# Kernel tuning notes

Hardware: AMD Instinct MI355X
Metric: run time of the kernel (lower is better)

Reference implementation:

```python
import jax, jax.numpy as jnp
import numpy as np

B, T, E = 2, 2048, 2048
H, HKV, M = 16, 4, 4
HD = E // H // M          # 32
NREP = H // HKV           # 4
EPS = 1e-5


def _rotary_interleaved(x, cos, sin):
    # x: (B, S, nh, HD); cos/sin: (S, HD//2), interleaved pairs (0::2, 1::2)
    x1 = x[..., 0::2]
    x2 = x[..., 1::2]
    c = cos[None, :, None, :]
    s = sin[None, :, None, :]
    o1 = x1 * c - x2 * s
    o2 = x1 * s + x2 * c
    return jnp.stack([o1, o2], axis=-1).reshape(x.shape)


def setup_inputs() -> dict:
    key = jax.random.key(0)
    ks = jax.random.split(key, 6)
    x = jax.random.normal(ks[0], (B, T, E), jnp.float32)
    pos = jnp.arange(T, dtype=jnp.float32)
    inv_freq = 1.0 / (10000.0 ** (jnp.arange(0, HD, 2, dtype=jnp.float32) / HD))
    ang = pos[:, None] * inv_freq[None, :]  # (T, HD//2)
    cos = jnp.cos(ang)
    sin = jnp.sin(ang)
    s = 0.02
    q_w = jax.random.normal(ks[1], (E, E), jnp.float32) * s
    k_w = jax.random.normal(ks[2], (E // NREP, E), jnp.float32) * s
    v_w = jax.random.normal(ks[3], (E // NREP, E), jnp.float32) * s
    out_w = jax.random.normal(ks[4], (E, E), jnp.float32) * s
    raw_map_weights = jnp.array([0.1 * (-1.0) ** i for i in range(M)], jnp.float32)
    weight_scale = jnp.ones((1,), jnp.float32)
    gamma = jnp.ones((M * HD,), jnp.float32)
    return dict(x=x, cos=cos, sin=sin, q_w=q_w, k_w=k_w, v_w=v_w, out_w=out_w,
                raw_map_weights=raw_map_weights, weight_scale=weight_scale, gamma=gamma)


def reference(x, cos, sin, q_w, k_w, v_w, out_w, raw_map_weights, weight_scale, gamma):
    # projections
    q = (x @ q_w.T).reshape(B, T, M * H, HD)
    k = (x @ k_w.T).reshape(B, T, M * HKV, HD)
    v = (x @ v_w.T).reshape(B, T, HKV, M * HD)
    # rotary (interleaved) on full head_dim, then split heads x maps (heads major, maps minor)
    q = _rotary_interleaved(q, cos, sin).reshape(B, T, H, M, HD)
    k = _rotary_interleaved(k, cos, sin).reshape(B, T, HKV, M, HD)
    # GQA: q head h attends to kv head h // NREP  (repeat_interleave semantics)
    k_rep = jnp.repeat(k, NREP, axis=2)  # (B,T,H,M,HD)
    v_rep = jnp.repeat(v, NREP, axis=2)  # (B,T,H,M*HD)
    map_w = jnp.tanh(raw_map_weights) * weight_scale[0]
    scale = HD ** -0.5  # flash_attn default softmax scale
    causal = jnp.tril(jnp.ones((T, T), dtype=bool))
    combined = jnp.zeros((B, T, H, M * HD), x.dtype)
    for i in range(M):  # small fixed num_maps loop
        scores = jnp.einsum('bqhd,bkhd->bhqk', q[:, :, :, i], k_rep[:, :, :, i]) * scale
        scores = jnp.where(causal[None, None], scores, -jnp.inf)
        p = jax.nn.softmax(scores, axis=-1)
        attn_i = jnp.einsum('bhqk,bkhe->bqhe', p, v_rep)  # (B,T,H,M*HD)
        combined = combined + map_w[i] * attn_i
    # RMSNorm over last dim (num_maps * head_dim) with affine weight
    var = jnp.mean(combined * combined, axis=-1, keepdims=True)
    normed = combined * jax.lax.rsqrt(var + EPS) * gamma
    out = normed.reshape(B, T, E) @ out_w.T
    return out
```

## Files before the change

kernel.cpp:

```cpp
#include <hip/hip_runtime.h>


typedef unsigned short u16;
typedef unsigned int u32;
typedef _Float16 f16;
typedef _Float16 f16x8 __attribute__((ext_vector_type(8)));
typedef float f32x4 __attribute__((ext_vector_type(4)));

#define B_ 2
#define T_ 2048
#define E_ 2048
#define H_ 16
#define HKV_ 4
#define M_ 4
#define HD_ 32
#define SCALE_Q 0.2550348873f

#define GLOAD_LDS(g, l)                                                   \
  __builtin_amdgcn_global_load_lds(                                       \
      (const __attribute__((address_space(1))) u32*)(g),                  \
      (__attribute__((address_space(3))) u32*)(l), 16, 0, 0)

__device__ __forceinline__ u16 f2h(float f) {
  f16 h = (f16)f;
  return __builtin_bit_cast(u16, h);
}

__global__ void cvt_all(const float* __restrict__ x, const float* __restrict__ qw,
                        const float* __restrict__ kw, const float* __restrict__ vw,
                        const float* __restrict__ ow, u16* __restrict__ xb,
                        u16* __restrict__ wcat, u16* __restrict__ wo16) {
  const float* src;
  u16* dst;
  int n4;
  switch (blockIdx.y) {
    case 0: src = x;  dst = xb;            n4 = 2097152; break;
    case 1: src = qw; dst = wcat;          n4 = 1048576; break;
    case 2: src = kw; dst = wcat + 4194304; n4 = 262144; break;
    case 3: src = vw; dst = wcat + 5242880; n4 = 262144; break;
    default: src = ow; dst = wo16;         n4 = 1048576; break;
  }
  int i = blockIdx.x * blockDim.x + threadIdx.x;
  if (i < n4) {
    float4 v = ((const float4*)src)[i];
    ushort4 o;
    o.x = f2h(v.x); o.y = f2h(v.y); o.z = f2h(v.z); o.w = f2h(v.w);
    ((ushort4*)dst)[i] = o;
  }
}

#define GEMM_CORE(A_, B_ptr, K_)                                              \
  for (int k0 = 0; k0 < (K_); k0 += 32) {                                     \
    _Pragma("unroll") for (int j = 0; j < 2; ++j) {                           \
      GLOAD_LDS(&(A_)[(size_t)(m0 + r0 + j * 64) * (K_) + k0 + c8],           \
                &As[tid * 8 + j * 2048]);                                     \
      GLOAD_LDS(&(B_ptr)[(size_t)(n0 + r0 + j * 64) * (K_) + k0 + c8],        \
                &Bs[tid * 8 + j * 2048]);                                     \
    }                                                                         \
    __syncthreads();                                                          \
    f16x8 af[4], bfr[4];                                                      \
    _Pragma("unroll") for (int mt = 0; mt < 4; ++mt)                          \
        af[mt] = *(const f16x8*)&As[(wm + mt * 16 + r) * 32 + g * 8];         \
    _Pragma("unroll") for (int nt = 0; nt < 4; ++nt)                          \
        bfr[nt] = *(const f16x8*)&Bs[(wn + nt * 16 + r) * 32 + g * 8];        \
    _Pragma("unroll") for (int mt = 0; mt < 4; ++mt)                          \
        _Pragma("unroll") for (int nt = 0; nt < 4; ++nt)                      \
            acc[mt][nt] = __builtin_amdgcn_mfma_f32_16x16x32_f16(             \
                af[mt], bfr[nt], acc[mt][nt], 0, 0, 0);                       \
    __syncthreads();                                                          \
  }

__global__ __launch_bounds__(256) void gemm_bt(const u16* __restrict__ A,
                                               const u16* __restrict__ Bm,
                                               float* __restrict__ C,
                                               int M, int N, int K) {
  __shared__ __align__(16) u16 As[128 * 32];
  __shared__ __align__(16) u16 Bs[128 * 32];
  const int tid = threadIdx.x;
  const int lane = tid & 63;
  const int wv = tid >> 6;
  const int g = lane >> 4;
  const int r = lane & 15;
  const int m0 = blockIdx.y * 128;
  const int n0 = blockIdx.x * 128;
  const int wm = (wv >> 1) * 64;
  const int wn = (wv & 1) * 64;
  f32x4 acc[4][4];
#pragma unroll
  for (int a = 0; a < 4; ++a)
#pragma unroll
    for (int b = 0; b < 4; ++b) acc[a][b] = (f32x4){0.f, 0.f, 0.f, 0.f};
  const int r0 = tid >> 2;
  const int c8 = (tid & 3) << 3;

  GEMM_CORE(A, Bm, K)

#pragma unroll
  for (int mt = 0; mt < 4; ++mt)
#pragma unroll
    for (int nt = 0; nt < 4; ++nt) {
      int row = m0 + wm + mt * 16 + g * 4;
      int col = n0 + wn + nt * 16 + r;
#pragma unroll
      for (int rr = 0; rr < 4; ++rr)
        C[(size_t)(row + rr) * N + col] = acc[mt][nt][rr];
    }
}

__global__ __launch_bounds__(256) void gemm_qkv_rope(
    const u16* __restrict__ A, const u16* __restrict__ Bm,
    const float* __restrict__ cosb, const float* __restrict__ sinb,
    u16* __restrict__ qp, u16* __restrict__ kp, u16* __restrict__ vtp) {
  __shared__ __align__(16) u16 As[128 * 32];
  __shared__ __align__(16) u16 Bs[128 * 32];
  const int tid = threadIdx.x;
  const int lane = tid & 63;
  const int wv = tid >> 6;
  const int g = lane >> 4;
  const int r = lane & 15;
  const int m0 = blockIdx.y * 128;
  const int n0 = blockIdx.x * 128;
  const int wm = (wv >> 1) * 64;
  const int wn = (wv & 1) * 64;
  f32x4 acc[4][4];
#pragma unroll
  for (int a = 0; a < 4; ++a)
#pragma unroll
    for (int b = 0; b < 4; ++b) acc[a][b] = (f32x4){0.f, 0.f, 0.f, 0.f};
  const int r0 = tid >> 2;
  const int c8 = (tid & 3) << 3;

  GEMM_CORE(A, Bm, 2048)

  const int b = m0 >> 11;
  const float signf = (r & 1) ? 1.f : -1.f;
  const int jb = r >> 1;

  if (n0 < 2048) {
#pragma unroll
    for (int mt = 0; mt < 4; ++mt) {
      int row = m0 + wm + mt * 16 + g * 4;
      int t0 = row & 2047;
#pragma unroll
      for (int rr = 0; rr < 4; ++rr) {
        int t = t0 + rr;
        float c0 = cosb[t * 16 + jb], s0 = sinb[t * 16 + jb];
        float c1 = cosb[t * 16 + 8 + jb], s1 = sinb[t * 16 + 8 + jb];
#pragma unroll
        for (int nt = 0; nt < 4; ++nt) {
          float xv = acc[mt][nt][rr];
          float pv = __shfl_xor(xv, 1, 64);
          float c = (nt & 1) ? c1 : c0;
          float s = (nt & 1) ? s1 : s0;
          float o = (xv * c + signf * pv * s) * SCALE_Q;
          int col = n0 + wn + nt * 16 + r;
          int hh = col >> 7, mm = (col >> 5) & 3, d = col & 31;
          qp[((((size_t)b * H_ + hh) * M_ + mm) * T_ + t) * HD_ + d] = f2h(o);
        }
      }
    }
  } else if (n0 < 2560) {
#pragma unroll
    for (int mt = 0; mt < 4; ++mt) {
      int row = m0 + wm + mt * 16 + g * 4;
      int t0 = row & 2047;
#pragma unroll
      for (int rr = 0; rr < 4; ++rr) {
        int t = t0 + rr;
        float c0 = cosb[t * 16 + jb], s0 = sinb[t * 16 + jb];
        float c1 = cosb[t * 16 + 8 + jb], s1 = sinb[t * 16 + 8 + jb];
#pragma unroll
        for (int nt = 0; nt < 4; ++nt) {
          float xv = acc[mt][nt][rr];
          float pv = __shfl_xor(xv, 1, 64);
          float c = (nt & 1) ? c1 : c0;
          float s = (nt & 1) ? s1 : s0;
          float o = xv * c + signf * pv * s;
          int col2 = n0 + wn + nt * 16 + r - 2048;
          int hh = col2 >> 7, mm = (col2 >> 5) & 3, d = col2 & 31;
          kp[((((size_t)b * HKV_ + hh) * M_ + mm) * T_ + t) * HD_ + d] = f2h(o);
        }
      }
    }
  } else {
#pragma unroll
    for (int mt = 0; mt < 4; ++mt) {
      int row = m0 + wm + mt * 16 + g * 4;
      int t0 = row & 2047;
#pragma unroll
      for (int nt = 0; nt < 4; ++nt) {
        int col3 = n0 + wn + nt * 16 + r - 2560;
        int hkv = col3 >> 7, e = col3 & 127;
        ushort4 w;
        w.x = f2h(acc[mt][nt][0]);
        w.y = f2h(acc[mt][nt][1]);
        w.z = f2h(acc[mt][nt][2]);
        w.w = f2h(acc[mt][nt][3]);
        *(ushort4*)&vtp[(((size_t)b * HKV_ + hkv) * 128 + e) * T_ + t0] = w;
      }
    }
  }
}

__global__ __launch_bounds__(256) void lstats_kernel(
    const u16* __restrict__ qp, const u16* __restrict__ kp,
    const float* __restrict__ rawW, const float* __restrict__ wscale,
    float* __restrict__ invw) {
  const int tid = threadIdx.x;
  const int lane = tid & 63;
  const int wv = tid >> 6;
  const int g = lane >> 4, r = lane & 15;
  const int h = blockIdx.y;
  const int b = blockIdx.z >> 2, e = blockIdx.z & 3;
  const int hkv = h >> 2;
  const int s0 = blockIdx.x * 4 + wv;

  const size_t qb = (((size_t)b * H_ + h) * M_ + e) * T_ * HD_;
  const size_t kb = (((size_t)b * HKV_ + hkv) * M_ + e) * T_ * HD_;
  const float mw = tanhf(rawW[e]) * wscale[0];

  for (int ps = 0; ps < 2; ++ps) {
    const int strip = ps ? 127 - s0 : s0;
    const int q0 = strip * 16;
    f16x8 qf = *(const f16x8*)&qp[qb + (size_t)(q0 + r) * HD_ + g * 8];
    float lacc[4] = {0.f, 0.f, 0.f, 0.f};

    for (int k0 = 0; k0 < q0 + 16; k0 += 64) {
      f32x4 s[4];
#pragma unroll
      for (int nt = 0; nt < 4; ++nt) {
        f16x8 kf = *(const f16x8*)&kp[kb + (size_t)(k0 + nt * 16 + r) * HD_ + g * 8];
        s[nt] = __builtin_amdgcn_mfma_f32_16x16x32_f16(qf, kf, (f32x4){0.f, 0.f, 0.f, 0.f}, 0, 0, 0);
      }
#pragma unroll
      for (int rr = 0; rr < 4; ++rr) {
        int row = q0 + g * 4 + rr;
#pragma unroll
        for (int nt = 0; nt < 4; ++nt) {
          int col = k0 + nt * 16 + r;
          float sv = (col <= row) ? s[nt][rr] : -1e30f;
          lacc[rr] += exp2f(sv);
        }
      }
    }
#pragma unroll
    for (int rr = 0; rr < 4; ++rr) {
      float l = lacc[rr];
#pragma unroll
      for (int off = 8; off >= 1; off >>= 1) l += __shfl_xor(l, off, 64);
      if (r == 0)
        invw[(((size_t)b * H_ + h) * M_ + e) * T_ + q0 + g * 4 + rr] = mw / l;
    }
  }
}

__global__ __launch_bounds__(256) void attn_kernel(
    const u16* __restrict__ qp, const u16* __restrict__ kp,
    const u16* __restrict__ vtp, const float* __restrict__ invw,
    const float* __restrict__ gamma, u16* __restrict__ normed) {
  __shared__ __align__(16) char smem[41984];
  u16* Ks = (u16*)smem;
  u16* Pc = (u16*)(smem + 32768);
  float* comb = (float*)smem;

  const int tid = threadIdx.x;
  const int lane = tid & 63;
  const int wv = tid >> 6;
  const int g = lane >> 4;
  const int r = lane & 15;
  const int h = blockIdx.y;
  const int b = blockIdx.z;
  const int hkv = h >> 2;

  const size_t qb = ((size_t)b * H_ + h) * M_ * T_ * HD_;
  const size_t kb = ((size_t)b * HKV_ + hkv) * M_ * T_ * HD_;
  const size_t vb = ((size_t)b * HKV_ + hkv) * 128 * (size_t)T_;

#define STAGE_KS(K0, DST)                                                     \
  {                                                                           \
    _Pragma("unroll") for (int j = 0; j < 4; ++j) {                           \
      int f = tid + j * 256;                                                  \
      int e_ = f >> 8, g2 = (f >> 6) & 3, kk = f & 63;                        \
      GLOAD_LDS(&kp[kb + ((size_t)e_ * T_ + (K0) + kk) * HD_ + g2 * 8],       \
                &(DST)[f * 8]);                                               \
    }                                                                         \
  }

  for (int ps = 0; ps < 2; ++ps) {
    const int q0 = (ps ? 31 - blockIdx.x : blockIdx.x) * 64;
    const int rq = q0 + wv * 16;

    f16x8 qf[4];
    float iw[4][4];
#pragma unroll
    for (int e = 0; e < 4; ++e) {
      qf[e] = *(const f16x8*)&qp[qb + ((size_t)e * T_ + rq + r) * HD_ + g * 8];
      const float* ivp = invw + (((size_t)b * H_ + h) * M_ + e) * T_;
#pragma unroll
      for (int rr = 0; rr < 4; ++rr) iw[e][rr] = ivp[rq + g * 4 + rr];
    }

    f32x4 acc[8];
#pragma unroll
    for (int ct = 0; ct < 8; ++ct) acc[ct] = (f32x4){0.f, 0.f, 0.f, 0.f};

    __syncthreads();
    STAGE_KS(0, Ks);
    __syncthreads();

    const int niter = q0 / 64 + 1;
    for (int i = 0; i < niter; ++i) {
      const int k0 = i * 64;
      u16* kbuf = Ks + (size_t)(i & 1) * 8192;
      if (i + 1 < niter) STAGE_KS(k0 + 64, Ks + (size_t)((i + 1) & 1) * 8192);

      f16x8 vf[2][8];
#pragma unroll
      for (int ct = 0; ct < 8; ++ct)
#pragma unroll
        for (int k2 = 0; k2 < 2; ++k2)
          vf[k2][ct] = *(const f16x8*)&vtp[vb + (size_t)(ct * 16 + r) * T_ + k0 + k2 * 32 + g * 8];

      float pc[4][4];
#pragma unroll
      for (int nt = 0; nt < 4; ++nt)
#pragma unroll
        for (int rr = 0; rr < 4; ++rr) pc[nt][rr] = 0.f;
      const bool need_mask = (k0 + 63 > rq);
#pragma unroll
      for (int e = 0; e < 4; ++e) {
        f32x4 s[4];
#pragma unroll
        for (int nt = 0; nt < 4; ++nt) {
          f16x8 kf = *(const f16x8*)&kbuf[e * 2048 + g * 512 + (nt * 16 + r) * 8];
          s[nt] = __builtin_amdgcn_mfma_f32_16x16x32_f16(qf[e], kf, (f32x4){0.f, 0.f, 0.f, 0.f}, 0, 0, 0);
        }
#pragma unroll
        for (int nt = 0; nt < 4; ++nt)
#pragma unroll
          for (int rr = 0; rr < 4; ++rr) {
            float sv = s[nt][rr];
            if (need_mask && (k0 + nt * 16 + r > rq + g * 4 + rr)) sv = -1e30f;
            pc[nt][rr] = fmaf(exp2f(sv), iw[e][rr], pc[nt][rr]);
          }
      }

      u16* myP = Pc + wv * (16 * 72);
#pragma unroll
      for (int nt = 0; nt < 4; ++nt)
#pragma unroll
        for (int rr = 0; rr < 4; ++rr)
          myP[(g * 4 + rr) * 72 + nt * 16 + r] = f2h(pc[nt][rr]);

      f16x8 pf[2];
#pragma unroll
      for (int k2 = 0; k2 < 2; ++k2)
        pf[k2] = *(const f16x8*)&myP[r * 72 + k2 * 32 + g * 8];

#pragma unroll
      for (int ct = 0; ct < 8; ++ct) {
        acc[ct] = __builtin_amdgcn_mfma_f32_16x16x32_f16(pf[0], vf[0][ct], acc[ct], 0, 0, 0);
        acc[ct] = __builtin_amdgcn_mfma_f32_16x16x32_f16(pf[1], vf[1][ct], acc[ct], 0, 0, 0);
      }

      __syncthreads();
    }

#pragma unroll
    for (int ct = 0; ct < 8; ++ct)
#pragma unroll
      for (int rr = 0; rr < 4; ++rr)
        comb[(wv * 16 + g * 4 + rr) * 132 + ct * 16 + r] = acc[ct][rr];
    __syncthreads();

    {
      int row = tid >> 2;
      int ch = (tid & 3) * 32;
      float vals[32];
      float ss = 0.f;
#pragma unroll
      for (int e2 = 0; e2 < 32; ++e2) {
        float v = comb[row * 132 + ch + e2];
        vals[e2] = v;
        ss += v * v;
      }
      ss += __shfl_xor(ss, 1, 64);
      ss += __shfl_xor(ss, 2, 64);
      float rstd = rsqrtf(ss * (1.f / 128.f) + 1e-5f);
      size_t obase = ((size_t)b * T_ + q0 + row) * E_ + (size_t)h * 128 + ch;
      union { u16 u[32]; uint4 q[4]; } pk;
#pragma unroll
      for (int e2 = 0; e2 < 32; ++e2)
        pk.u[e2] = f2h(vals[e2] * rstd * gamma[ch + e2]);
#pragma unroll
      for (int qq = 0; qq < 4; ++qq)
        *(uint4*)&normed[obase + qq * 8] = pk.q[qq];
    }
  }
#undef STAGE_KS
}

extern "C" void kernel_launch(void* const* d_in, const int* in_sizes, int n_in,
                              void* d_out, int out_size, void* d_ws, size_t ws_size,
                              hipStream_t stream) {
  const float* x = (const float*)d_in[0];
  const float* cosb = (const float*)d_in[1];
  const float* sinb = (const float*)d_in[2];
  const float* qw = (const float*)d_in[3];
  const float* kw = (const float*)d_in[4];
  const float* vw = (const float*)d_in[5];
  const float* ow = (const float*)d_in[6];
  const float* rawW = (const float*)d_in[7];
  const float* wsc = (const float*)d_in[8];
  const float* gm = (const float*)d_in[9];
  float* out = (float*)d_out;

  char* ws = (char*)d_ws;
  u16* xb = (u16*)(ws);
  u16* wcat = (u16*)(ws + (16ull << 20));
  u16* wo16 = (u16*)(ws + (28ull << 20));
  float* invw = (float*)(ws + (36ull << 20));
  u16* qp = (u16*)(ws + (84ull << 20));
  u16* kp = (u16*)(ws + (100ull << 20));
  u16* vtp = (u16*)(ws + (104ull << 20));
  u16* normed = xb;

  cvt_all<<<dim3(8192, 5), 256, 0, stream>>>(x, qw, kw, vw, ow, xb, wcat, wo16);
  gemm_qkv_rope<<<dim3(24, 32), 256, 0, stream>>>(xb, wcat, cosb, sinb, qp, kp, vtp);
  lstats_kernel<<<dim3(16, H_, B_ * M_), 256, 0, stream>>>(qp, kp, rawW, wsc, invw);
  attn_kernel<<<dim3(16, H_, B_), 256, 0, stream>>>(qp, kp, vtp, invw, gm, normed);
  gemm_bt<<<dim3(2048 / 128, 4096 / 128), 256, 0, stream>>>(normed, wo16, out, 4096, 2048, 2048);
}
```

Baseline: 515.7 us.

## Split attention key range across two waves with 16-row query strips

The attention kernel now runs 128-thread blocks over 16-row query strips, with the two waves splitting each 64-key chunk into 32-key halves. Their partial outputs are summed in LDS before the RMSNorm. The K tile is no longer staged through LDS with double buffering; each wave reads K directly from global memory, which cuts shared memory use and the per-iteration barriers so more blocks fit per CU. The stats kernel also skips mask evaluation on fully unmasked chunks. The trade-offs are more redundant global K/V loads per block and less reuse of each K tile across query rows.

```diff
diff --git a/kernel.cpp b/kernel.cpp
--- a/kernel.cpp
+++ b/kernel.cpp
@@ -232,15 +232,22 @@
         f16x8 kf = *(const f16x8*)&kp[kb + (size_t)(k0 + nt * 16 + r) * HD_ + g * 8];
         s[nt] = __builtin_amdgcn_mfma_f32_16x16x32_f16(qf, kf, (f32x4){0.f, 0.f, 0.f, 0.f}, 0, 0, 0);
       }
-#pragma unroll
-      for (int rr = 0; rr < 4; ++rr) {
-        int row = q0 + g * 4 + rr;
-#pragma unroll
-        for (int nt = 0; nt < 4; ++nt) {
-          int col = k0 + nt * 16 + r;
-          float sv = (col <= row) ? s[nt][rr] : -1e30f;
-          lacc[rr] += exp2f(sv);
+      if (k0 + 63 > q0) {
+#pragma unroll
+        for (int rr = 0; rr < 4; ++rr) {
+          int row = q0 + g * 4 + rr;
+#pragma unroll
+          for (int nt = 0; nt < 4; ++nt) {
+            int col = k0 + nt * 16 + r;
+            float sv = (col <= row) ? s[nt][rr] : -1e30f;
+            lacc[rr] += exp2f(sv);
+          }
         }
+      } else {
+#pragma unroll
+        for (int rr = 0; rr < 4; ++rr)
+#pragma unroll
+          for (int nt = 0; nt < 4; ++nt) lacc[rr] += exp2f(s[nt][rr]);
       }
     }
 #pragma unroll
@@ -254,14 +261,13 @@
   }
 }
 
-__global__ __launch_bounds__(256) void attn_kernel(
+__global__ __launch_bounds__(128, 4) void attn_kernel(
     const u16* __restrict__ qp, const u16* __restrict__ kp,
     const u16* __restrict__ vtp, const float* __restrict__ invw,
     const float* __restrict__ gamma, u16* __restrict__ normed) {
-  __shared__ __align__(16) char smem[41984];
-  u16* Ks = (u16*)smem;
-  u16* Pc = (u16*)(smem + 32768);
-  float* comb = (float*)smem;
+  __shared__ __align__(16) char smem[19200];
+  u16* Pc = (u16*)smem;
+  float* comb = (float*)(smem + 2304);
 
   const int tid = threadIdx.x;
   const int lane = tid & 63;
@@ -276,94 +282,68 @@
   const size_t kb = ((size_t)b * HKV_ + hkv) * M_ * T_ * HD_;
   const size_t vb = ((size_t)b * HKV_ + hkv) * 128 * (size_t)T_;
 
-#define STAGE_KS(K0, DST)                                                     \
-  {                                                                           \
-    _Pragma("unroll") for (int j = 0; j < 4; ++j) {                           \
-      int f = tid + j * 256;                                                  \
-      int e_ = f >> 8, g2 = (f >> 6) & 3, kk = f & 63;                        \
-      GLOAD_LDS(&kp[kb + ((size_t)e_ * T_ + (K0) + kk) * HD_ + g2 * 8],       \
-                &(DST)[f * 8]);                                               \
-    }                                                                         \
-  }
-
   for (int ps = 0; ps < 2; ++ps) {
-    const int q0 = (ps ? 31 - blockIdx.x : blockIdx.x) * 64;
-    const int rq = q0 + wv * 16;
+    const int q0 = (ps ? 127 - blockIdx.x : blockIdx.x) * 16;
 
     f16x8 qf[4];
     float iw[4][4];
 #pragma unroll
     for (int e = 0; e < 4; ++e) {
-      qf[e] = *(const f16x8*)&qp[qb + ((size_t)e * T_ + rq + r) * HD_ + g * 8];
+      qf[e] = *(const f16x8*)&qp[qb + ((size_t)e * T_ + q0 + r) * HD_ + g * 8];
       const float* ivp = invw + (((size_t)b * H_ + h) * M_ + e) * T_;
 #pragma unroll
-      for (int rr = 0; rr < 4; ++rr) iw[e][rr] = ivp[rq + g * 4 + rr];
+      for (int rr = 0; rr < 4; ++rr) iw[e][rr] = ivp[q0 + g * 4 + rr];
     }
 
     f32x4 acc[8];
 #pragma unroll
     for (int ct = 0; ct < 8; ++ct) acc[ct] = (f32x4){0.f, 0.f, 0.f, 0.f};
-
-    __syncthreads();
-    STAGE_KS(0, Ks);
-    __syncthreads();
 
     const int niter = q0 / 64 + 1;
     for (int i = 0; i < niter; ++i) {
-      const int k0 = i * 64;
-      u16* kbuf = Ks + (size_t)(i & 1) * 8192;
-      if (i + 1 < niter) STAGE_KS(k0 + 64, Ks + (size_t)((i + 1) & 1) * 8192);
-
-      f16x8 vf[2][8];
+      const int k0 = i * 64 + wv * 32;
+      if (k0 > q0 + 15) continue;
+
+      f16x8 vf[8];
 #pragma unroll
       for (int ct = 0; ct < 8; ++ct)
-#pragma unroll
-        for (int k2 = 0; k2 < 2; ++k2)
-          vf[k2][ct] = *(const f16x8*)&vtp[vb + (size_t)(ct * 16 + r) * T_ + k0 + k2 * 32 + g * 8];
-
-      float pc[4][4];
-#pragma unroll
-      for (int nt = 0; nt < 4; ++nt)
+        vf[ct] = *(const f16x8*)&vtp[vb + (size_t)(ct * 16 + r) * T_ + k0 + g * 8];
+
+      float pc[2][4];
+#pragma unroll
+      for (int nt = 0; nt < 2; ++nt)
 #pragma unroll
         for (int rr = 0; rr < 4; ++rr) pc[nt][rr] = 0.f;
-      const bool need_mask = (k0 + 63 > rq);
+      const bool need_mask = (k0 + 31 > q0);
 #pragma unroll
       for (int e = 0; e < 4; ++e) {
-        f32x4 s[4];
-#pragma unroll
-        for (int nt = 0; nt < 4; ++nt) {
-          f16x8 kf = *(const f16x8*)&kbuf[e * 2048 + g * 512 + (nt * 16 + r) * 8];
+        f32x4 s[2];
+#pragma unroll
+        for (int nt = 0; nt < 2; ++nt) {
+          f16x8 kf = *(const f16x8*)&kp[kb + ((size_t)e * T_ + k0 + nt * 16 + r) * HD_ + g * 8];
           s[nt] = __builtin_amdgcn_mfma_f32_16x16x32_f16(qf[e], kf, (f32x4){0.f, 0.f, 0.f, 0.f}, 0, 0, 0);
         }
 #pragma unroll
-        for (int nt = 0; nt < 4; ++nt)
+        for (int nt = 0; nt < 2; ++nt)
 #pragma unroll
           for (int rr = 0; rr < 4; ++rr) {
             float sv = s[nt][rr];
-            if (need_mask && (k0 + nt * 16 + r > rq + g * 4 + rr)) sv = -1e30f;
+            if (need_mask && (k0 + nt * 16 + r > q0 + g * 4 + rr)) sv = -1e30f;
             pc[nt][rr] = fmaf(exp2f(sv), iw[e][rr], pc[nt][rr]);
           }
       }
 
-      u16* myP = Pc + wv * (16 * 72);
-#pragma unroll
-      for (int nt = 0; nt < 4; ++nt)
+      u16* myP = Pc + wv * 576;
+#pragma unroll
+      for (int nt = 0; nt < 2; ++nt)
 #pragma unroll
         for (int rr = 0; rr < 4; ++rr)
-          myP[(g * 4 + rr) * 72 + nt * 16 + r] = f2h(pc[nt][rr]);
-
-      f16x8 pf[2];
-#pragma unroll
-      for (int k2 = 0; k2 < 2; ++k2)
-        pf[k2] = *(const f16x8*)&myP[r * 72 + k2 * 32 + g * 8];
-
-#pragma unroll
-      for (int ct = 0; ct < 8; ++ct) {
-        acc[ct] = __builtin_amdgcn_mfma_f32_16x16x32_f16(pf[0], vf[0][ct], acc[ct], 0, 0, 0);
-        acc[ct] = __builtin_amdgcn_mfma_f32_16x16x32_f16(pf[1], vf[1][ct], acc[ct], 0, 0, 0);
-      }
-
-      __syncthreads();
+          myP[(g * 4 + rr) * 36 + nt * 16 + r] = f2h(pc[nt][rr]);
+      f16x8 pf = *(const f16x8*)&myP[r * 36 + g * 8];
+
+#pragma unroll
+      for (int ct = 0; ct < 8; ++ct)
+        acc[ct] = __builtin_amdgcn_mfma_f32_16x16x32_f16(pf, vf[ct], acc[ct], 0, 0, 0);
     }
 
 #pragma unroll
@@ -374,30 +354,30 @@
     __syncthreads();
 
     {
-      int row = tid >> 2;
-      int ch = (tid & 3) * 32;
-      float vals[32];
+      int row = tid >> 3;
+      int ch = (tid & 7) * 16;
+      float vals[16];
       float ss = 0.f;
 #pragma unroll
-      for (int e2 = 0; e2 < 32; ++e2) {
-        float v = comb[row * 132 + ch + e2];
+      for (int e2 = 0; e2 < 16; ++e2) {
+        float v = comb[row * 132 + ch + e2] + comb[(16 + row) * 132 + ch + e2];
         vals[e2] = v;
         ss += v * v;
       }
       ss += __shfl_xor(ss, 1, 64);
       ss += __shfl_xor(ss, 2, 64);
+      ss += __shfl_xor(ss, 4, 64);
       float rstd = rsqrtf(ss * (1.f / 128.f) + 1e-5f);
       size_t obase = ((size_t)b * T_ + q0 + row) * E_ + (size_t)h * 128 + ch;
-      union { u16 u[32]; uint4 q[4]; } pk;
-#pragma unroll
-      for (int e2 = 0; e2 < 32; ++e2)
+      union { u16 u[16]; uint4 q[2]; } pk;
+#pragma unroll
+      for (int e2 = 0; e2 < 16; ++e2)
         pk.u[e2] = f2h(vals[e2] * rstd * gamma[ch + e2]);
-#pragma unroll
-      for (int qq = 0; qq < 4; ++qq)
-        *(uint4*)&normed[obase + qq * 8] = pk.q[qq];
-    }
-  }
-#undef STAGE_KS
+      *(uint4*)&normed[obase] = pk.q[0];
+      *(uint4*)&normed[obase + 8] = pk.q[1];
+    }
+    __syncthreads();
+  }
 }
 
 extern "C" void kernel_launch(void* const* d_in, const int* in_sizes, int n_in,
@@ -428,6 +408,6 @@
   cvt_all<<<dim3(8192, 5), 256, 0, stream>>>(x, qw, kw, vw, ow, xb, wcat, wo16);
   gemm_qkv_rope<<<dim3(24, 32), 256, 0, stream>>>(xb, wcat, cosb, sinb, qp, kp, vtp);
   lstats_kernel<<<dim3(16, H_, B_ * M_), 256, 0, stream>>>(qp, kp, rawW, wsc, invw);
-  attn_kernel<<<dim3(16, H_, B_), 256, 0, stream>>>(qp, kp, vtp, invw, gm, normed);
+  attn_kernel<<<dim3(64, H_, B_), 128, 0, stream>>>(qp, kp, vtp, invw, gm, normed);
   gemm_bt<<<dim3(2048 / 128, 4096 / 128), 256, 0, stream>>>(normed, wo16, out, 4096, 2048, 2048);
 }
```

New measurement: 539.7 us. +4.7%, slower.
